# Kernel tuning notes

Hardware: AMD Instinct MI355X
Metric: run time of the kernel (lower is better)

Reference implementation:

```python
import jax, jax.numpy as jnp
import numpy as np

B, S, D, H = 2, 4096, 512, 8
DH = D // H
EPS = 1e-5


def setup_inputs() -> dict:
    key = jax.random.key(0)
    ks = jax.random.split(key, 8)
    s = 0.02
    return {
        "x": jax.random.normal(ks[0], (B, S, D), jnp.float32),
        "in_proj_w": jax.random.normal(ks[1], (3 * D, D), jnp.float32) * s,
        "in_proj_b": jnp.zeros((3 * D,), jnp.float32),
        "out_proj_w": jax.random.normal(ks[2], (D, D), jnp.float32) * s,
        "out_proj_b": jnp.zeros((D,), jnp.float32),
        "ln1_g": jnp.ones((D,), jnp.float32),
        "ln1_b": jnp.zeros((D,), jnp.float32),
        "ln2_g": jnp.ones((D,), jnp.float32),
        "ln2_b": jnp.zeros((D,), jnp.float32),
        "w1": jax.random.normal(ks[3], (D, D), jnp.float32) * s,
        "b1": jnp.zeros((D,), jnp.float32),
        "w2": jax.random.normal(ks[4], (D, D), jnp.float32) * s,
        "b2": jnp.zeros((D,), jnp.float32),
        "window": 256,
    }


def _layernorm(x, g, b):
    mu = jnp.mean(x, axis=-1, keepdims=True)
    var = jnp.mean(jnp.square(x - mu), axis=-1, keepdims=True)
    return (x - mu) * jax.lax.rsqrt(var + EPS) * g + b


def reference(x, in_proj_w, in_proj_b, out_proj_w, out_proj_b,
              ln1_g, ln1_b, ln2_g, ln2_b, w1, b1, w2, b2, window):
    b, s, d = x.shape
    # sliding-window mask: allowed iff |i - j| <= window
    idx = jnp.arange(s)
    allowed = jnp.abs(idx[:, None] - idx[None, :]) <= window  # [S,S]

    # fused QKV projection (torch MultiheadAttention layout: W [3D, D])
    qkv = x @ in_proj_w.T + in_proj_b  # [B,S,3D]
    q, k, v = jnp.split(qkv, 3, axis=-1)
    q = q.reshape(b, s, H, DH)
    k = k.reshape(b, s, H, DH)
    v = v.reshape(b, s, H, DH)

    scale = 1.0 / jnp.sqrt(jnp.float32(DH))
    scores = jnp.einsum("bqhd,bkhd->bhqk", q, k) * scale  # [B,H,S,S]
    scores = jnp.where(allowed[None, None], scores, -jnp.inf)
    attn = jax.nn.softmax(scores, axis=-1)
    ctx = jnp.einsum("bhqk,bkhd->bqhd", attn, v).reshape(b, s, d)
    attn_out = ctx @ out_proj_w.T + out_proj_b

    # residual + LayerNorm (dropout rate 0 -> identity)
    h = _layernorm(x + attn_out, ln1_g, ln1_b)
    mlp = jax.nn.relu(h @ w1.T + b1) @ w2.T + b2
    return _layernorm(h + mlp, ln2_g, ln2_b)
```

## Files before the change

kernel.cpp:

```cpp
#include <hip/hip_runtime.h>

typedef __bf16 bf16;
typedef __bf16 bf16x2 __attribute__((ext_vector_type(2)));
typedef __bf16 bf16x8 __attribute__((ext_vector_type(8)));
typedef float f32x4 __attribute__((ext_vector_type(4)));

#define S_LEN 4096
#define DMODEL 512
#define NHEAD 8
#define DHEAD 64
#define BATCH 2
#define M_ROWS (BATCH * S_LEN)
#define K_DIM 512
#define QKV_LD 1536

__device__ __forceinline__ void async16(void* lds, const void* g) {
  __builtin_amdgcn_global_load_lds(
      (const __attribute__((address_space(1))) unsigned int*)g,
      (__attribute__((address_space(3))) unsigned int*)lds, 16, 0, 0);
}

__global__ void detect_dtype(const unsigned int* __restrict__ x,
                             int* __restrict__ flag) {
  const int lane = threadIdx.x;
  int cnt = 0;
#pragma unroll
  for (int i = 0; i < 16; ++i) {
    const unsigned int w = x[lane * 16 + i];
    const unsigned int e = (w >> 7) & 0xFFu;
    cnt += (e >= 100u && e <= 140u) ? 1 : 0;
  }
#pragma unroll
  for (int off = 1; off < 64; off <<= 1) cnt += __shfl_xor(cnt, off);
  if (lane == 0) *flag = (cnt >= 700) ? 1 : 0;
}

__device__ __forceinline__ bf16x8 ld8(const void* p, size_t e, bool asF32) {
  if (asF32) {
    const float* q = (const float*)p + e;
    const float4 a = *(const float4*)q;
    const float4 b = *(const float4*)(q + 4);
    bf16x8 r;
    r[0] = (bf16)a.x; r[1] = (bf16)a.y; r[2] = (bf16)a.z; r[3] = (bf16)a.w;
    r[4] = (bf16)b.x; r[5] = (bf16)b.y; r[6] = (bf16)b.z; r[7] = (bf16)b.w;
    return r;
  }
  return *(const bf16x8*)((const bf16*)p + e);
}

__device__ __forceinline__ float ld1(const void* p, size_t e, bool asF32) {
  return asF32 ? ((const float*)p)[e] : (float)((const bf16*)p)[e];
}

__global__ __launch_bounds__(256) void cvt_all(const void* __restrict__ x,
                                               const void* __restrict__ s0,
                                               const void* __restrict__ s1,
                                               const void* __restrict__ s2,
                                               const void* __restrict__ s3,
                                               bf16* __restrict__ xb,
                                               bf16* __restrict__ warena,
                                               const int* __restrict__ flag) {
  const bool f32in = (*flag == 0);
  const int b = blockIdx.x;
  if (b < 2048) {
    const size_t idx = ((size_t)b * 256 + threadIdx.x) * 8;
    *(bf16x8*)(xb + idx) = ld8(x, idx, f32in);
    return;
  }
  const int wb = b - 2048;
  const void* s;
  size_t doff;
  int lb;
  if (wb < 384)      { s = s0; doff = 0;        lb = wb; }
  else if (wb < 512) { s = s1; doff = 786432;   lb = wb - 384; }
  else if (wb < 640) { s = s2; doff = 1048576;  lb = wb - 512; }
  else               { s = s3; doff = 1310720;  lb = wb - 640; }
  const size_t idx = (size_t)lb * 2048 + threadIdx.x * 8;
  *(bf16x8*)(warena + doff + idx) = ld8(s, idx, f32in);
}

template <int NMAT, int BN, bool RELU>
__global__ __launch_bounds__(256) void gemm_bt(const bf16* __restrict__ A,
                                               const bf16* __restrict__ W,
                                               const void* __restrict__ bias,
                                               bf16* __restrict__ C,
                                               const int* __restrict__ flag) {
  __shared__ __align__(16) bf16 As[128 * 64];
  __shared__ __align__(16) bf16 Ws[BN * 64];

  const bool f32in = (*flag == 0);

  const int t = threadIdx.x;
  const int lane = t & 63;
  const int wave = t >> 6;
  constexpr int MT = (BN == 128) ? 4 : 2;
  const int wm = (BN == 128) ? (wave >> 1) * 64 : wave * 32;
  const int wn = (BN == 128) ? (wave & 1) * 64 : 0;
  const int l16 = lane & 15;
  const int quad = lane >> 4;

  constexpr int NB = NMAT / BN;
  constexpr int MPX = (M_ROWS / 128) / 8;
  const int bid = blockIdx.x;
  const int xcd = bid & 7;
  const int r = bid >> 3;
  const int m0 = (xcd * MPX + r / NB) * 128;
  const int n0 = (r % NB) * BN;

  const int rr = lane >> 3;
  const int cb = (lane & 7) ^ rr;
  const int sw = l16 & 7;

  f32x4 acc[MT][4];
#pragma unroll
  for (int i = 0; i < MT; ++i)
#pragma unroll
    for (int j = 0; j < 4; ++j) acc[i][j] = (f32x4){0.f, 0.f, 0.f, 0.f};

  for (int kt = 0; kt < K_DIM; kt += 64) {
    __syncthreads();
#pragma unroll
    for (int i = 0; i < 4; ++i) {
      const int r0 = wave * 32 + i * 8;
      async16(&As[r0 * 64], &A[(size_t)(m0 + r0 + rr) * K_DIM + kt + cb * 8]);
    }
#pragma unroll
    for (int i = 0; i < BN / 32; ++i) {
      const int r0 = wave * (BN / 4) + i * 8;
      async16(&Ws[r0 * 64], &W[(size_t)(n0 + r0 + rr) * K_DIM + kt + cb * 8]);
    }
    __syncthreads();
#pragma unroll
    for (int ks = 0; ks < 2; ++ks) {
      bf16x8 af[MT], wf[4];
#pragma unroll
      for (int mt = 0; mt < MT; ++mt)
        af[mt] = *(const bf16x8*)&As[(wm + mt * 16 + l16) * 64 +
                                     (((ks * 4 + quad) ^ sw) * 8)];
#pragma unroll
      for (int nt = 0; nt < 4; ++nt)
        wf[nt] = *(const bf16x8*)&Ws[(wn + nt * 16 + l16) * 64 +
                                     (((ks * 4 + quad) ^ sw) * 8)];
#pragma unroll
      for (int mt = 0; mt < MT; ++mt)
#pragma unroll
        for (int nt = 0; nt < 4; ++nt)
          acc[mt][nt] = __builtin_amdgcn_mfma_f32_16x16x32_bf16(af[mt], wf[nt],
                                                                acc[mt][nt], 0, 0, 0);
    }
  }

#pragma unroll
  for (int nt = 0; nt < 4; ++nt) {
    const int n = n0 + wn + nt * 16 + l16;
    const float bv = ld1(bias, n, f32in);
#pragma unroll
    for (int mt = 0; mt < MT; ++mt) {
#pragma unroll
      for (int r4 = 0; r4 < 4; ++r4) {
        const int m = m0 + wm + mt * 16 + quad * 4 + r4;
        float v = acc[mt][nt][r4] + bv;
        if (RELU) v = fmaxf(v, 0.f);
        C[(size_t)m * NMAT + n] = (bf16)v;
      }
    }
  }
}

__global__ __launch_bounds__(256) void attn_fwd(const bf16* __restrict__ qkv,
                                                bf16* __restrict__ ctx,
                                                const int* __restrict__ wptr) {
  __shared__ __align__(16) bf16 Kt[2][64 * 64];
  __shared__ __align__(16) bf16 Vt[2][64][72];
  __shared__ __align__(16) bf16 Pbuf[4][16][72];

  const int t = threadIdx.x;
  const int lane = t & 63;
  const int wave = t >> 6;
  const int l16 = lane & 15;
  const int quad = lane >> 4;
  const int rr = lane >> 3;
  const int cb = (lane & 7) ^ rr;
  const int sw = l16 & 7;

  const int bid = blockIdx.x;
  const int xcd = bid & 7;
  const int jj = bid >> 3;
  const int pair = xcd * 2 + (jj >> 6);
  const int qblk = jj & 63;
  const int h = pair & 7;
  const int b = pair >> 3;
  const int qbase = qblk * 64;
  int window = *wptr;
  if (window < 0) window = 0;
  if (window > S_LEN) window = S_LEN;
  const float sc_log2e = 0.125f * 1.44269504f;

  const int qrow = qbase + wave * 16 + l16;
  const bf16* qp = qkv + (size_t)(b * S_LEN + qrow) * QKV_LD + h * DHEAD;
  const bf16x8 qf0 = *(const bf16x8*)(qp + quad * 8);
  const bf16x8 qf1 = *(const bf16x8*)(qp + 32 + quad * 8);

  f32x4 o[4];
#pragma unroll
  for (int nt = 0; nt < 4; ++nt) o[nt] = (f32x4){0.f, 0.f, 0.f, 0.f};
  float lp[4] = {0.f, 0.f, 0.f, 0.f};

  int kstart = qbase - window;
  if (kstart < 0) kstart = 0;
  kstart &= ~63;
  int kend = qbase + 64 + window;
  if (kend > S_LEN) kend = S_LEN;
  const int niter = (kend - kstart + 63) >> 6;

  const int vk = (t & 31) * 2;
  const int vd = (t >> 5) * 8;
  const bf16* vbase = qkv + (size_t)(b * S_LEN) * QKV_LD + 2 * DMODEL + h * DHEAD + vd;
  const bf16* kbase = qkv + (size_t)(b * S_LEN) * QKV_LD + DMODEL + h * DHEAD;

#pragma unroll
  for (int i = 0; i < 2; ++i) {
    const int r0 = wave * 16 + i * 8;
    async16(&Kt[0][r0 * 64],
            &kbase[(size_t)(kstart + r0 + rr) * QKV_LD + cb * 8]);
  }
  {
    const bf16* p = vbase + (size_t)(kstart + vk) * QKV_LD;
    const bf16x8 va = *(const bf16x8*)p;
    const bf16x8 vb = *(const bf16x8*)(p + QKV_LD);
#pragma unroll
    for (int j = 0; j < 8; ++j) {
      bf16x2 pr; pr[0] = va[j]; pr[1] = vb[j];
      *(bf16x2*)&Vt[0][vd + j][vk] = pr;
    }
  }

  for (int it = 0; it < niter; ++it) {
    const int kt = kstart + it * 64;
    const int cur = it & 1;
    __syncthreads();

    bf16x8 na, nb;
    const bool have_next = (it + 1 < niter);
    if (have_next) {
#pragma unroll
      for (int i = 0; i < 2; ++i) {
        const int r0 = wave * 16 + i * 8;
        async16(&Kt[cur ^ 1][r0 * 64],
                &kbase[(size_t)(kt + 64 + r0 + rr) * QKV_LD + cb * 8]);
      }
      const bf16* p = vbase + (size_t)(kt + 64 + vk) * QKV_LD;
      na = *(const bf16x8*)p;
      nb = *(const bf16x8*)(p + QKV_LD);
    }

    f32x4 s[4];
#pragma unroll
    for (int t4 = 0; t4 < 4; ++t4) s[t4] = (f32x4){0.f, 0.f, 0.f, 0.f};
#pragma unroll
    for (int t4 = 0; t4 < 4; ++t4) {
      const int row = t4 * 16 + l16;
      const bf16x8 k0 = *(const bf16x8*)&Kt[cur][row * 64 + ((quad ^ sw) * 8)];
      const bf16x8 k1 =
          *(const bf16x8*)&Kt[cur][row * 64 + (((4 + quad) ^ sw) * 8)];
      s[t4] = __builtin_amdgcn_mfma_f32_16x16x32_bf16(qf0, k0, s[t4], 0, 0, 0);
      s[t4] = __builtin_amdgcn_mfma_f32_16x16x32_bf16(qf1, k1, s[t4], 0, 0, 0);
    }

#pragma unroll
    for (int r = 0; r < 4; ++r) {
      const int q = qbase + wave * 16 + quad * 4 + r;
      const int lo = q - window, hi = q + window;
      float psum = 0.f;
#pragma unroll
      for (int t4 = 0; t4 < 4; ++t4) {
        const int key = kt + t4 * 16 + l16;
        const float p = (key >= lo && key <= hi)
                            ? __builtin_amdgcn_exp2f(s[t4][r] * sc_log2e)
                            : 0.f;
        psum += p;
        Pbuf[wave][quad * 4 + r][t4 * 16 + l16] = (bf16)p;
      }
      lp[r] += psum;
    }

    const bf16x8 pf0 = *(const bf16x8*)&Pbuf[wave][l16][quad * 8];
    const bf16x8 pf1 = *(const bf16x8*)&Pbuf[wave][l16][32 + quad * 8];
#pragma unroll
    for (int nt = 0; nt < 4; ++nt) {
      const bf16x8 v0 = *(const bf16x8*)&Vt[cur][nt * 16 + l16][quad * 8];
      const bf16x8 v1 = *(const bf16x8*)&Vt[cur][nt * 16 + l16][32 + quad * 8];
      o[nt] = __builtin_amdgcn_mfma_f32_16x16x32_bf16(pf0, v0, o[nt], 0, 0, 0);
      o[nt] = __builtin_amdgcn_mfma_f32_16x16x32_bf16(pf1, v1, o[nt], 0, 0, 0);
    }

    if (have_next) {
#pragma unroll
      for (int j = 0; j < 8; ++j) {
        bf16x2 pr; pr[0] = na[j]; pr[1] = nb[j];
        *(bf16x2*)&Vt[cur ^ 1][vd + j][vk] = pr;
      }
    }
  }

#pragma unroll
  for (int r = 0; r < 4; ++r) {
#pragma unroll
    for (int off = 1; off < 16; off <<= 1) lp[r] += __shfl_xor(lp[r], off);
    const float inv = (lp[r] > 0.f) ? (1.0f / lp[r]) : 0.f;
    const int q = qbase + wave * 16 + quad * 4 + r;
#pragma unroll
    for (int nt = 0; nt < 4; ++nt) {
      ctx[(size_t)(b * S_LEN + q) * DMODEL + h * DHEAD + nt * 16 + l16] =
          (bf16)(o[nt][r] * inv);
    }
  }
}

template <bool A_RAW, bool OUT_RAW>
__global__ __launch_bounds__(256) void ln_fused(const void* __restrict__ a,
                                                const bf16* __restrict__ bres,
                                                const void* __restrict__ g,
                                                const void* __restrict__ be,
                                                void* __restrict__ out,
                                                const int* __restrict__ flag) {
  const bool f32in = (*flag == 0);
  const int row = blockIdx.x * 4 + (threadIdx.x >> 6);
  const int lane = threadIdx.x & 63;
  const size_t base = (size_t)row * DMODEL + lane * 8;
  const bf16x8 va = ld8(a, base, A_RAW && f32in);
  const bf16x8 vb = *(const bf16x8*)(bres + base);
  float v[8], s = 0.f, s2 = 0.f;
#pragma unroll
  for (int j = 0; j < 8; ++j) {
    v[j] = (float)va[j] + (float)vb[j];
    s += v[j];
    s2 += v[j] * v[j];
  }
#pragma unroll
  for (int off = 1; off < 64; off <<= 1) {
    s += __shfl_xor(s, off);
    s2 += __shfl_xor(s2, off);
  }
  const float mean = s * (1.0f / DMODEL);
  float var = s2 * (1.0f / DMODEL) - mean * mean;
  if (var < 0.f) var = 0.f;
  const float rstd = rsqrtf(var + 1e-5f);
  const bf16x8 gv = ld8(g, lane * 8, f32in);
  const bf16x8 bev = ld8(be, lane * 8, f32in);
  float ov[8];
#pragma unroll
  for (int j = 0; j < 8; ++j)
    ov[j] = (v[j] - mean) * rstd * (float)gv[j] + (float)bev[j];
  if (OUT_RAW && f32in) {
    float4 o0 = {ov[0], ov[1], ov[2], ov[3]};
    float4 o1 = {ov[4], ov[5], ov[6], ov[7]};
    *(float4*)((float*)out + base) = o0;
    *(float4*)((float*)out + base + 4) = o1;
  } else {
    bf16x8 ob;
#pragma unroll
    for (int j = 0; j < 8; ++j) ob[j] = (bf16)ov[j];
    *(bf16x8*)((bf16*)out + base) = ob;
  }
}

extern "C" void kernel_launch(void* const* d_in, const int* in_sizes, int n_in,
                              void* d_out, int out_size, void* d_ws, size_t ws_size,
                              hipStream_t stream) {
  const void* x          = d_in[0];
  const void* in_proj_w  = d_in[1];
  const void* in_proj_b  = d_in[2];
  const void* out_proj_w = d_in[3];
  const void* out_proj_b = d_in[4];
  const void* ln1_g      = d_in[5];
  const void* ln1_b      = d_in[6];
  const void* ln2_g      = d_in[7];
  const void* ln2_b      = d_in[8];
  const void* w1         = d_in[9];
  const void* b1         = d_in[10];
  const void* w2         = d_in[11];
  const void* b2         = d_in[12];
  const int*  wptr       = (const int*)d_in[13];

  char* ws = (char*)d_ws;
  int* flag = (int*)ws;
  bf16* warena = (bf16*)(ws + 256);
  bf16* wq = warena;
  bf16* wo = warena + 786432;
  bf16* w1b = warena + 1048576;
  bf16* w2b = warena + 1310720;
  char* big = ws + 256 + 3145728;
  bf16* qkv      = (bf16*)big;
  bf16* h        = (bf16*)big;
  bf16* a1       = (bf16*)(big + 8388608);
  bf16* attn_out = (bf16*)(big + 16777216);
  bf16* mlp      = attn_out;
  bf16* xb       = (bf16*)d_out;
  bf16* ctx      = (bf16*)d_out;

  detect_dtype<<<1, 64, 0, stream>>>((const unsigned int*)x, flag);
  cvt_all<<<2816, 256, 0, stream>>>(x, in_proj_w, out_proj_w, w1, w2, xb, warena, flag);
  gemm_bt<QKV_LD, 128, false><<<768, 256, 0, stream>>>(
      xb, wq, in_proj_b, qkv, flag);
  attn_fwd<<<dim3(BATCH * NHEAD * (S_LEN / 64)), 256, 0, stream>>>(qkv, ctx, wptr);
  gemm_bt<DMODEL, 64, false><<<512, 256, 0, stream>>>(
      ctx, wo, out_proj_b, attn_out, flag);
  ln_fused<true, false><<<dim3(M_ROWS / 4), 256, 0, stream>>>(
      x, attn_out, ln1_g, ln1_b, h, flag);
  gemm_bt<DMODEL, 64, true><<<512, 256, 0, stream>>>(
      h, w1b, b1, a1, flag);
  gemm_bt<DMODEL, 64, false><<<512, 256, 0, stream>>>(
      a1, w2b, b2, mlp, flag);
  ln_fused<false, true><<<dim3(M_ROWS / 4), 256, 0, stream>>>(
      h, mlp, ln2_g, ln2_b, d_out, flag);
}
```

Baseline: 205.5 us.

## Fuse out-proj, LN1, MLP and LN2 into one tail kernel; split QKV layout

```diff
diff --git a/kernel.cpp b/kernel.cpp
--- a/kernel.cpp
+++ b/kernel.cpp
@@ -12,7 +12,7 @@
 #define BATCH 2
 #define M_ROWS (BATCH * S_LEN)
 #define K_DIM 512
-#define QKV_LD 1536
+#define QLD 512
 
 __device__ __forceinline__ void async16(void* lds, const void* g) {
   __builtin_amdgcn_global_load_lds(
@@ -20,9 +20,7 @@
       (__attribute__((address_space(3))) unsigned int*)lds, 16, 0, 0);
 }
 
-__global__ void detect_dtype(const unsigned int* __restrict__ x,
-                             int* __restrict__ flag) {
-  const int lane = threadIdx.x;
+__device__ __forceinline__ int detect_bf16(const unsigned int* x, int lane) {
   int cnt = 0;
 #pragma unroll
   for (int i = 0; i < 16; ++i) {
@@ -32,7 +30,7 @@
   }
 #pragma unroll
   for (int off = 1; off < 64; off <<= 1) cnt += __shfl_xor(cnt, off);
-  if (lane == 0) *flag = (cnt >= 700) ? 1 : 0;
+  return (cnt >= 700) ? 1 : 0;
 }
 
 __device__ __forceinline__ bf16x8 ld8(const void* p, size_t e, bool asF32) {
@@ -59,9 +57,11 @@
                                                const void* __restrict__ s3,
                                                bf16* __restrict__ xb,
                                                bf16* __restrict__ warena,
-                                               const int* __restrict__ flag) {
-  const bool f32in = (*flag == 0);
+                                               int* __restrict__ flag) {
+  const int isbf = detect_bf16((const unsigned int*)x, threadIdx.x & 63);
+  const bool f32in = (isbf == 0);
   const int b = blockIdx.x;
+  if (b == 0 && threadIdx.x == 0) *flag = isbf;
   if (b < 2048) {
     const size_t idx = ((size_t)b * 256 + threadIdx.x) * 8;
     *(bf16x8*)(xb + idx) = ld8(x, idx, f32in);
@@ -79,41 +79,37 @@
   *(bf16x8*)(warena + doff + idx) = ld8(s, idx, f32in);
 }
 
-template <int NMAT, int BN, bool RELU>
-__global__ __launch_bounds__(256) void gemm_bt(const bf16* __restrict__ A,
-                                               const bf16* __restrict__ W,
-                                               const void* __restrict__ bias,
-                                               bf16* __restrict__ C,
-                                               const int* __restrict__ flag) {
+__global__ __launch_bounds__(256) void gemm_qkv(const bf16* __restrict__ A,
+                                                const bf16* __restrict__ W,
+                                                const void* __restrict__ bias,
+                                                bf16* __restrict__ C,
+                                                const int* __restrict__ flag) {
   __shared__ __align__(16) bf16 As[128 * 64];
-  __shared__ __align__(16) bf16 Ws[BN * 64];
+  __shared__ __align__(16) bf16 Ws[128 * 64];
 
   const bool f32in = (*flag == 0);
-
   const int t = threadIdx.x;
   const int lane = t & 63;
   const int wave = t >> 6;
-  constexpr int MT = (BN == 128) ? 4 : 2;
-  const int wm = (BN == 128) ? (wave >> 1) * 64 : wave * 32;
-  const int wn = (BN == 128) ? (wave & 1) * 64 : 0;
+  const int wm = (wave >> 1) * 64;
+  const int wn = (wave & 1) * 64;
   const int l16 = lane & 15;
   const int quad = lane >> 4;
 
-  constexpr int NB = NMAT / BN;
-  constexpr int MPX = (M_ROWS / 128) / 8;
+  constexpr int NB = 1536 / 128;
   const int bid = blockIdx.x;
   const int xcd = bid & 7;
   const int r = bid >> 3;
-  const int m0 = (xcd * MPX + r / NB) * 128;
-  const int n0 = (r % NB) * BN;
+  const int m0 = (xcd * 8 + r / NB) * 128;
+  const int n0 = (r % NB) * 128;
 
   const int rr = lane >> 3;
   const int cb = (lane & 7) ^ rr;
   const int sw = l16 & 7;
 
-  f32x4 acc[MT][4];
-#pragma unroll
-  for (int i = 0; i < MT; ++i)
+  f32x4 acc[4][4];
+#pragma unroll
+  for (int i = 0; i < 4; ++i)
 #pragma unroll
     for (int j = 0; j < 4; ++j) acc[i][j] = (f32x4){0.f, 0.f, 0.f, 0.f};
 
@@ -125,16 +121,16 @@
       async16(&As[r0 * 64], &A[(size_t)(m0 + r0 + rr) * K_DIM + kt + cb * 8]);
     }
 #pragma unroll
-    for (int i = 0; i < BN / 32; ++i) {
-      const int r0 = wave * (BN / 4) + i * 8;
+    for (int i = 0; i < 4; ++i) {
+      const int r0 = wave * 32 + i * 8;
       async16(&Ws[r0 * 64], &W[(size_t)(n0 + r0 + rr) * K_DIM + kt + cb * 8]);
     }
     __syncthreads();
 #pragma unroll
     for (int ks = 0; ks < 2; ++ks) {
-      bf16x8 af[MT], wf[4];
-#pragma unroll
-      for (int mt = 0; mt < MT; ++mt)
+      bf16x8 af[4], wf[4];
+#pragma unroll
+      for (int mt = 0; mt < 4; ++mt)
         af[mt] = *(const bf16x8*)&As[(wm + mt * 16 + l16) * 64 +
                                      (((ks * 4 + quad) ^ sw) * 8)];
 #pragma unroll
@@ -142,7 +138,7 @@
         wf[nt] = *(const bf16x8*)&Ws[(wn + nt * 16 + l16) * 64 +
                                      (((ks * 4 + quad) ^ sw) * 8)];
 #pragma unroll
-      for (int mt = 0; mt < MT; ++mt)
+      for (int mt = 0; mt < 4; ++mt)
 #pragma unroll
         for (int nt = 0; nt < 4; ++nt)
           acc[mt][nt] = __builtin_amdgcn_mfma_f32_16x16x32_bf16(af[mt], wf[nt],
@@ -154,25 +150,28 @@
   for (int nt = 0; nt < 4; ++nt) {
     const int n = n0 + wn + nt * 16 + l16;
     const float bv = ld1(bias, n, f32in);
-#pragma unroll
-    for (int mt = 0; mt < MT; ++mt) {
+    bf16* Cm = C + (size_t)(n >> 9) * ((size_t)M_ROWS * DMODEL) + (n & 511);
+#pragma unroll
+    for (int mt = 0; mt < 4; ++mt) {
 #pragma unroll
       for (int r4 = 0; r4 < 4; ++r4) {
         const int m = m0 + wm + mt * 16 + quad * 4 + r4;
-        float v = acc[mt][nt][r4] + bv;
-        if (RELU) v = fmaxf(v, 0.f);
-        C[(size_t)m * NMAT + n] = (bf16)v;
-      }
-    }
-  }
-}
-
-__global__ __launch_bounds__(256) void attn_fwd(const bf16* __restrict__ qkv,
-                                                bf16* __restrict__ ctx,
+        Cm[(size_t)m * DMODEL] = (bf16)(acc[mt][nt][r4] + bv);
+      }
+    }
+  }
+}
+
+__global__ __launch_bounds__(256) void attn_fwd(bf16* __restrict__ qkv,
                                                 const int* __restrict__ wptr) {
   __shared__ __align__(16) bf16 Kt[2][64 * 64];
   __shared__ __align__(16) bf16 Vt[2][64][72];
   __shared__ __align__(16) bf16 Pbuf[4][16][72];
+
+  const bf16* Q = qkv;
+  const bf16* K = qkv + (size_t)M_ROWS * DMODEL;
+  const bf16* V = qkv + 2 * (size_t)M_ROWS * DMODEL;
+  bf16* ctxw = qkv;
 
   const int t = threadIdx.x;
   const int lane = t & 63;
@@ -197,7 +196,7 @@
   const float sc_log2e = 0.125f * 1.44269504f;
 
   const int qrow = qbase + wave * 16 + l16;
-  const bf16* qp = qkv + (size_t)(b * S_LEN + qrow) * QKV_LD + h * DHEAD;
+  const bf16* qp = Q + (size_t)(b * S_LEN + qrow) * QLD + h * DHEAD;
   const bf16x8 qf0 = *(const bf16x8*)(qp + quad * 8);
   const bf16x8 qf1 = *(const bf16x8*)(qp + 32 + quad * 8);
 
@@ -215,19 +214,19 @@
 
   const int vk = (t & 31) * 2;
   const int vd = (t >> 5) * 8;
-  const bf16* vbase = qkv + (size_t)(b * S_LEN) * QKV_LD + 2 * DMODEL + h * DHEAD + vd;
-  const bf16* kbase = qkv + (size_t)(b * S_LEN) * QKV_LD + DMODEL + h * DHEAD;
+  const bf16* vbase = V + (size_t)(b * S_LEN) * QLD + h * DHEAD + vd;
+  const bf16* kbase = K + (size_t)(b * S_LEN) * QLD + h * DHEAD;
 
 #pragma unroll
   for (int i = 0; i < 2; ++i) {
     const int r0 = wave * 16 + i * 8;
     async16(&Kt[0][r0 * 64],
-            &kbase[(size_t)(kstart + r0 + rr) * QKV_LD + cb * 8]);
+            &kbase[(size_t)(kstart + r0 + rr) * QLD + cb * 8]);
   }
   {
-    const bf16* p = vbase + (size_t)(kstart + vk) * QKV_LD;
+    const bf16* p = vbase + (size_t)(kstart + vk) * QLD;
     const bf16x8 va = *(const bf16x8*)p;
-    const bf16x8 vb = *(const bf16x8*)(p + QKV_LD);
+    const bf16x8 vb = *(const bf16x8*)(p + QLD);
 #pragma unroll
     for (int j = 0; j < 8; ++j) {
       bf16x2 pr; pr[0] = va[j]; pr[1] = vb[j];
@@ -247,16 +246,18 @@
       for (int i = 0; i < 2; ++i) {
         const int r0 = wave * 16 + i * 8;
         async16(&Kt[cur ^ 1][r0 * 64],
-                &kbase[(size_t)(kt + 64 + r0 + rr) * QKV_LD + cb * 8]);
-      }
-      const bf16* p = vbase + (size_t)(kt + 64 + vk) * QKV_LD;
+                &kbase[(size_t)(kt + 64 + r0 + rr) * QLD + cb * 8]);
+      }
+      const bf16* p = vbase + (size_t)(kt + 64 + vk) * QLD;
       na = *(const bf16x8*)p;
-      nb = *(const bf16x8*)(p + QKV_LD);
+      nb = *(const bf16x8*)(p + QLD);
     }
 
     f32x4 s[4];
 #pragma unroll
     for (int t4 = 0; t4 < 4; ++t4) s[t4] = (f32x4){0.f, 0.f, 0.f, 0.f};
+
+    __builtin_amdgcn_s_setprio(1);
 #pragma unroll
     for (int t4 = 0; t4 < 4; ++t4) {
       const int row = t4 * 16 + l16;
@@ -266,26 +267,26 @@
       s[t4] = __builtin_amdgcn_mfma_f32_16x16x32_bf16(qf0, k0, s[t4], 0, 0, 0);
       s[t4] = __builtin_amdgcn_mfma_f32_16x16x32_bf16(qf1, k1, s[t4], 0, 0, 0);
     }
+    __builtin_amdgcn_s_setprio(0);
 
 #pragma unroll
     for (int r = 0; r < 4; ++r) {
       const int q = qbase + wave * 16 + quad * 4 + r;
       const int lo = q - window, hi = q + window;
-      float psum = 0.f;
 #pragma unroll
       for (int t4 = 0; t4 < 4; ++t4) {
         const int key = kt + t4 * 16 + l16;
         const float p = (key >= lo && key <= hi)
                             ? __builtin_amdgcn_exp2f(s[t4][r] * sc_log2e)
                             : 0.f;
-        psum += p;
+        lp[r] += p;
         Pbuf[wave][quad * 4 + r][t4 * 16 + l16] = (bf16)p;
       }
-      lp[r] += psum;
     }
 
     const bf16x8 pf0 = *(const bf16x8*)&Pbuf[wave][l16][quad * 8];
     const bf16x8 pf1 = *(const bf16x8*)&Pbuf[wave][l16][32 + quad * 8];
+    __builtin_amdgcn_s_setprio(1);
 #pragma unroll
     for (int nt = 0; nt < 4; ++nt) {
       const bf16x8 v0 = *(const bf16x8*)&Vt[cur][nt * 16 + l16][quad * 8];
@@ -293,6 +294,7 @@
       o[nt] = __builtin_amdgcn_mfma_f32_16x16x32_bf16(pf0, v0, o[nt], 0, 0, 0);
       o[nt] = __builtin_amdgcn_mfma_f32_16x16x32_bf16(pf1, v1, o[nt], 0, 0, 0);
     }
+    __builtin_amdgcn_s_setprio(0);
 
     if (have_next) {
 #pragma unroll
@@ -311,57 +313,268 @@
     const int q = qbase + wave * 16 + quad * 4 + r;
 #pragma unroll
     for (int nt = 0; nt < 4; ++nt) {
-      ctx[(size_t)(b * S_LEN + q) * DMODEL + h * DHEAD + nt * 16 + l16] =
+      ctxw[(size_t)(b * S_LEN + q) * QLD + h * DHEAD + nt * 16 + l16] =
           (bf16)(o[nt][r] * inv);
     }
   }
 }
 
-template <bool A_RAW, bool OUT_RAW>
-__global__ __launch_bounds__(256) void ln_fused(const void* __restrict__ a,
-                                                const bf16* __restrict__ bres,
-                                                const void* __restrict__ g,
-                                                const void* __restrict__ be,
-                                                void* __restrict__ out,
-                                                const int* __restrict__ flag) {
+__global__ __launch_bounds__(512, 1) void fused_tail(
+    const bf16* __restrict__ ctxg, const void* __restrict__ x,
+    const bf16* __restrict__ wo, const bf16* __restrict__ w1m,
+    const bf16* __restrict__ w2m, const void* __restrict__ bo,
+    const void* __restrict__ g1, const void* __restrict__ be1,
+    const void* __restrict__ b1p, const void* __restrict__ b2p,
+    const void* __restrict__ g2, const void* __restrict__ be2,
+    void* __restrict__ out, const int* __restrict__ flag) {
+  __shared__ __align__(16) bf16 AL0[32 * 512];
+  __shared__ __align__(16) bf16 hL[32 * 512];
+  __shared__ __align__(16) bf16 Wslab[2][512 * 32];
+  float* red = (float*)AL0;
+
   const bool f32in = (*flag == 0);
-  const int row = blockIdx.x * 4 + (threadIdx.x >> 6);
-  const int lane = threadIdx.x & 63;
-  const size_t base = (size_t)row * DMODEL + lane * 8;
-  const bf16x8 va = ld8(a, base, A_RAW && f32in);
-  const bf16x8 vb = *(const bf16x8*)(bres + base);
-  float v[8], s = 0.f, s2 = 0.f;
-#pragma unroll
-  for (int j = 0; j < 8; ++j) {
-    v[j] = (float)va[j] + (float)vb[j];
-    s += v[j];
-    s2 += v[j] * v[j];
-  }
-#pragma unroll
-  for (int off = 1; off < 64; off <<= 1) {
-    s += __shfl_xor(s, off);
-    s2 += __shfl_xor(s2, off);
-  }
-  const float mean = s * (1.0f / DMODEL);
-  float var = s2 * (1.0f / DMODEL) - mean * mean;
-  if (var < 0.f) var = 0.f;
-  const float rstd = rsqrtf(var + 1e-5f);
-  const bf16x8 gv = ld8(g, lane * 8, f32in);
-  const bf16x8 bev = ld8(be, lane * 8, f32in);
-  float ov[8];
-#pragma unroll
-  for (int j = 0; j < 8; ++j)
-    ov[j] = (v[j] - mean) * rstd * (float)gv[j] + (float)bev[j];
-  if (OUT_RAW && f32in) {
-    float4 o0 = {ov[0], ov[1], ov[2], ov[3]};
-    float4 o1 = {ov[4], ov[5], ov[6], ov[7]};
-    *(float4*)((float*)out + base) = o0;
-    *(float4*)((float*)out + base + 4) = o1;
-  } else {
-    bf16x8 ob;
-#pragma unroll
-    for (int j = 0; j < 8; ++j) ob[j] = (bf16)ov[j];
-    *(bf16x8*)((bf16*)out + base) = ob;
+  const int t = threadIdx.x;
+  const int lane = t & 63;
+  const int wave = t >> 6;
+  const int l16 = lane & 15;
+  const int quad = lane >> 4;
+  const int wcol = wave * 64;
+  const int rowbase = blockIdx.x * 32;
+
+#pragma unroll
+  for (int j = 0; j < 4; ++j) {
+    const int dgi = j * 512 + t;
+    const int row = dgi >> 6, g = dgi & 63;
+    async16(&AL0[dgi * 8],
+            &ctxg[(size_t)(rowbase + row) * 512 + ((g ^ (row & 7)) * 8)]);
+  }
+  auto stageW = [&](int buf, int s) {
+    const bf16* wsrc = (s < 16) ? wo : (s < 32) ? w1m : w2m;
+    const int kt = (s & 15) * 32;
+#pragma unroll
+    for (int j = 0; j < 4; ++j) {
+      const int dgi = j * 512 + t;
+      const int n = dgi >> 2, g = dgi & 3;
+      async16(&Wslab[buf][dgi * 8],
+              &wsrc[(size_t)n * 512 + kt + ((g ^ ((n >> 1) & 3)) * 8)]);
+    }
+  };
+  stageW(0, 0);
+
+  f32x4 acc[2][4];
+  auto zeroAcc = [&]() {
+#pragma unroll
+    for (int mt = 0; mt < 2; ++mt)
+#pragma unroll
+      for (int ct = 0; ct < 4; ++ct) acc[mt][ct] = (f32x4){0.f, 0.f, 0.f, 0.f};
+  };
+  zeroAcc();
+
+  auto computeStep = [&](const bf16* AL, int s) {
+    const int gb = (s & 15) * 4;
+    bf16x8 af[2], wfv[4];
+#pragma unroll
+    for (int mt = 0; mt < 2; ++mt) {
+      const int row = mt * 16 + l16;
+      af[mt] = *(const bf16x8*)&AL[row * 512 + (((gb + quad) ^ (row & 7)) * 8)];
+    }
+    const bf16* WB = &Wslab[s & 1][0];
+#pragma unroll
+    for (int ct = 0; ct < 4; ++ct) {
+      const int n = wcol + ct * 16 + l16;
+      wfv[ct] = *(const bf16x8*)&WB[n * 32 + ((quad ^ ((n >> 1) & 3)) * 8)];
+    }
+#pragma unroll
+    for (int mt = 0; mt < 2; ++mt)
+#pragma unroll
+      for (int ct = 0; ct < 4; ++ct)
+        acc[mt][ct] = __builtin_amdgcn_mfma_f32_16x16x32_bf16(
+            af[mt], wfv[ct], acc[mt][ct], 0, 0, 0);
+  };
+
+  int s = 0;
+  for (int i = 0; i < 16; ++i, ++s) {
+    __syncthreads();
+    stageW((s + 1) & 1, s + 1);
+    computeStep(AL0, s);
+  }
+
+  float hreg[2][4][4];
+  {
+    float vv[2][4][4], ps[2][4], ps2[2][4];
+#pragma unroll
+    for (int mt = 0; mt < 2; ++mt)
+#pragma unroll
+      for (int r = 0; r < 4; ++r) { ps[mt][r] = 0.f; ps2[mt][r] = 0.f; }
+#pragma unroll
+    for (int mt = 0; mt < 2; ++mt)
+#pragma unroll
+      for (int ct = 0; ct < 4; ++ct) {
+        const int col = wcol + ct * 16 + l16;
+        const float bov = ld1(bo, col, f32in);
+#pragma unroll
+        for (int r = 0; r < 4; ++r) {
+          const int row = mt * 16 + quad * 4 + r;
+          const float xv = ld1(x, (size_t)(rowbase + row) * 512 + col, f32in);
+          const float v = acc[mt][ct][r] + bov + xv;
+          vv[mt][ct][r] = v;
+          ps[mt][r] += v;
+          ps2[mt][r] += v * v;
+        }
+      }
+#pragma unroll
+    for (int mt = 0; mt < 2; ++mt)
+#pragma unroll
+      for (int r = 0; r < 4; ++r)
+#pragma unroll
+        for (int off = 1; off < 16; off <<= 1) {
+          ps[mt][r] += __shfl_xor(ps[mt][r], off);
+          ps2[mt][r] += __shfl_xor(ps2[mt][r], off);
+        }
+    __syncthreads();
+    if (l16 == 0) {
+#pragma unroll
+      for (int mt = 0; mt < 2; ++mt)
+#pragma unroll
+        for (int r = 0; r < 4; ++r) {
+          const int row = mt * 16 + quad * 4 + r;
+          red[(row * 8 + wave) * 2 + 0] = ps[mt][r];
+          red[(row * 8 + wave) * 2 + 1] = ps2[mt][r];
+        }
+    }
+    __syncthreads();
+    float mean[2][4], rstd[2][4];
+#pragma unroll
+    for (int mt = 0; mt < 2; ++mt)
+#pragma unroll
+      for (int r = 0; r < 4; ++r) {
+        const int row = mt * 16 + quad * 4 + r;
+        float sm = 0.f, sq = 0.f;
+#pragma unroll
+        for (int w = 0; w < 8; ++w) {
+          sm += red[(row * 8 + w) * 2 + 0];
+          sq += red[(row * 8 + w) * 2 + 1];
+        }
+        const float mu = sm * (1.f / 512.f);
+        float var = sq * (1.f / 512.f) - mu * mu;
+        if (var < 0.f) var = 0.f;
+        mean[mt][r] = mu;
+        rstd[mt][r] = rsqrtf(var + 1e-5f);
+      }
+#pragma unroll
+    for (int mt = 0; mt < 2; ++mt)
+#pragma unroll
+      for (int ct = 0; ct < 4; ++ct) {
+        const int col = wcol + ct * 16 + l16;
+        const float gv = ld1(g1, col, f32in);
+        const float bv = ld1(be1, col, f32in);
+#pragma unroll
+        for (int r = 0; r < 4; ++r) {
+          const int row = mt * 16 + quad * 4 + r;
+          const float hv = (vv[mt][ct][r] - mean[mt][r]) * rstd[mt][r] * gv + bv;
+          hreg[mt][ct][r] = hv;
+          hL[row * 512 + (((col >> 3) ^ (row & 7)) * 8) + (col & 7)] = (bf16)hv;
+        }
+      }
+  }
+  zeroAcc();
+
+  for (int i = 0; i < 16; ++i, ++s) {
+    __syncthreads();
+    stageW((s + 1) & 1, s + 1);
+    computeStep(hL, s);
+  }
+  {
+#pragma unroll
+    for (int mt = 0; mt < 2; ++mt)
+#pragma unroll
+      for (int ct = 0; ct < 4; ++ct) {
+        const int col = wcol + ct * 16 + l16;
+        const float b1v = ld1(b1p, col, f32in);
+#pragma unroll
+        for (int r = 0; r < 4; ++r) {
+          const int row = mt * 16 + quad * 4 + r;
+          const float a = fmaxf(acc[mt][ct][r] + b1v, 0.f);
+          AL0[row * 512 + (((col >> 3) ^ (row & 7)) * 8) + (col & 7)] = (bf16)a;
+        }
+      }
+  }
+  zeroAcc();
+
+  for (int i = 0; i < 16; ++i, ++s) {
+    __syncthreads();
+    if (s + 1 < 48) stageW((s + 1) & 1, s + 1);
+    computeStep(AL0, s);
+  }
+  __syncthreads();
+
+  {
+    float vv[2][4][4], ps[2][4], ps2[2][4];
+#pragma unroll
+    for (int mt = 0; mt < 2; ++mt)
+#pragma unroll
+      for (int r = 0; r < 4; ++r) { ps[mt][r] = 0.f; ps2[mt][r] = 0.f; }
+#pragma unroll
+    for (int mt = 0; mt < 2; ++mt)
+#pragma unroll
+      for (int ct = 0; ct < 4; ++ct) {
+        const int col = wcol + ct * 16 + l16;
+        const float b2v = ld1(b2p, col, f32in);
+#pragma unroll
+        for (int r = 0; r < 4; ++r) {
+          const float v = acc[mt][ct][r] + b2v + hreg[mt][ct][r];
+          vv[mt][ct][r] = v;
+          ps[mt][r] += v;
+          ps2[mt][r] += v * v;
+        }
+      }
+#pragma unroll
+    for (int mt = 0; mt < 2; ++mt)
+#pragma unroll
+      for (int r = 0; r < 4; ++r)
+#pragma unroll
+        for (int off = 1; off < 16; off <<= 1) {
+          ps[mt][r] += __shfl_xor(ps[mt][r], off);
+          ps2[mt][r] += __shfl_xor(ps2[mt][r], off);
+        }
+    if (l16 == 0) {
+#pragma unroll
+      for (int mt = 0; mt < 2; ++mt)
+#pragma unroll
+        for (int r = 0; r < 4; ++r) {
+          const int row = mt * 16 + quad * 4 + r;
+          red[(row * 8 + wave) * 2 + 0] = ps[mt][r];
+          red[(row * 8 + wave) * 2 + 1] = ps2[mt][r];
+        }
+    }
+    __syncthreads();
+#pragma unroll
+    for (int mt = 0; mt < 2; ++mt)
+#pragma unroll
+      for (int r = 0; r < 4; ++r) {
+        const int row = mt * 16 + quad * 4 + r;
+        float sm = 0.f, sq = 0.f;
+#pragma unroll
+        for (int w = 0; w < 8; ++w) {
+          sm += red[(row * 8 + w) * 2 + 0];
+          sq += red[(row * 8 + w) * 2 + 1];
+        }
+        const float mu = sm * (1.f / 512.f);
+        float var = sq * (1.f / 512.f) - mu * mu;
+        if (var < 0.f) var = 0.f;
+        const float rs = rsqrtf(var + 1e-5f);
+#pragma unroll
+        for (int ct = 0; ct < 4; ++ct) {
+          const int col = wcol + ct * 16 + l16;
+          const float gv = ld1(g2, col, f32in);
+          const float bv = ld1(be2, col, f32in);
+          const float ov = (vv[mt][ct][r] - mu) * rs * gv + bv;
+          if (f32in)
+            ((float*)out)[(size_t)(rowbase + row) * 512 + col] = ov;
+          else
+            ((bf16*)out)[(size_t)(rowbase + row) * 512 + col] = (bf16)ov;
+        }
+      }
   }
 }
 
@@ -386,32 +599,17 @@
   char* ws = (char*)d_ws;
   int* flag = (int*)ws;
   bf16* warena = (bf16*)(ws + 256);
-  bf16* wq = warena;
-  bf16* wo = warena + 786432;
+  bf16* wq  = warena;
+  bf16* wo  = warena + 786432;
   bf16* w1b = warena + 1048576;
   bf16* w2b = warena + 1310720;
-  char* big = ws + 256 + 3145728;
-  bf16* qkv      = (bf16*)big;
-  bf16* h        = (bf16*)big;
-  bf16* a1       = (bf16*)(big + 8388608);
-  bf16* attn_out = (bf16*)(big + 16777216);
-  bf16* mlp      = attn_out;
-  bf16* xb       = (bf16*)d_out;
-  bf16* ctx      = (bf16*)d_out;
-
-  detect_dtype<<<1, 64, 0, stream>>>((const unsigned int*)x, flag);
+  bf16* qkvS = (bf16*)(ws + 256 + 3145728);
+  bf16* xb   = (bf16*)d_out;
+
   cvt_all<<<2816, 256, 0, stream>>>(x, in_proj_w, out_proj_w, w1, w2, xb, warena, flag);
-  gemm_bt<QKV_LD, 128, false><<<768, 256, 0, stream>>>(
-      xb, wq, in_proj_b, qkv, flag);
-  attn_fwd<<<dim3(BATCH * NHEAD * (S_LEN / 64)), 256, 0, stream>>>(qkv, ctx, wptr);
-  gemm_bt<DMODEL, 64, false><<<512, 256, 0, stream>>>(
-      ctx, wo, out_proj_b, attn_out, flag);
-  ln_fused<true, false><<<dim3(M_ROWS / 4), 256, 0, stream>>>(
-      x, attn_out, ln1_g, ln1_b, h, flag);
-  gemm_bt<DMODEL, 64, true><<<512, 256, 0, stream>>>(
-      h, w1b, b1, a1, flag);
-  gemm_bt<DMODEL, 64, false><<<512, 256, 0, stream>>>(
-      a1, w2b, b2, mlp, flag);
-  ln_fused<false, true><<<dim3(M_ROWS / 4), 256, 0, stream>>>(
-      h, mlp, ln2_g, ln2_b, d_out, flag);
-}
+  gemm_qkv<<<768, 256, 0, stream>>>(xb, wq, in_proj_b, qkvS, flag);
+  attn_fwd<<<dim3(BATCH * NHEAD * (S_LEN / 64)), 256, 0, stream>>>(qkvS, wptr);
+  fused_tail<<<256, 512, 0, stream>>>(qkvS, x, wo, w1b, w2b, out_proj_b,
+                                      ln1_g, ln1_b, b1, b2, ln2_g, ln2_b,
+                                      d_out, flag);
+}
```

Measured after the change: 208.7 us. Within noise of the previous version (+1.6%).
